# Kernel tuning notes

Measured on AMD Instinct MI355X. Metric: run time of the kernel, lower is better.

## Reference

```python
import jax, jax.numpy as jnp
import numpy as np

B, N, C, H = 4, 4096, 128, 4


def setup_inputs() -> dict:
    key = jax.random.key(0)
    ks = jax.random.split(key, 12)
    def rn(k, shape, s=0.02):
        return jax.random.normal(k, shape, jnp.float32) * s
    return dict(
        x=jax.random.normal(ks[0], (B, N, C), jnp.float32),
        p=jax.random.normal(ks[1], (B, N, 3), jnp.float32),
        fcl1_w=rn(ks[2], (C, C)), fcl1_b=jnp.zeros((C,), jnp.float32),
        # per-head (stacked over leading H axis) TransformerLayer params
        hq_w=rn(ks[3], (H, C, C)), hq_b=jnp.zeros((H, C), jnp.float32),
        hk_w=rn(ks[4], (H, C, C)), hk_b=jnp.zeros((H, C), jnp.float32),
        hv_w=rn(ks[5], (H, C, C)), hv_b=jnp.zeros((H, C), jnp.float32),
        pe1_w=rn(ks[6], (H, C, 3)), pe1_b=jnp.zeros((H, C), jnp.float32),  # Conv1d(3->C, k=1)
        pe2_w=rn(ks[7], (H, C, C)), pe2_b=jnp.zeros((H, C), jnp.float32),  # Conv1d(C->C, k=1)
        mh_w=rn(ks[8], (C, 4 * C)), mh_b=jnp.zeros((C,), jnp.float32),
        fcl2_w=rn(ks[9], (C, C)), fcl2_b=jnp.zeros((C,), jnp.float32),
    )


def reference(x, p, fcl1_w, fcl1_b, hq_w, hq_b, hk_w, hk_b, hv_w, hv_b,
              pe1_w, pe1_b, pe2_w, pe2_b, mh_w, mh_b, fcl2_w, fcl2_b):
    residual = x
    xf = x @ fcl1_w.T + fcl1_b  # fcl1
    scale = 1.0 / jnp.sqrt(jnp.asarray(C, jnp.float32))

    def head(qw, qb, kw, kb, vw, vb, p1w, p1b, p2w, p2b):
        # kernel-size-1 Conv1d == pointwise linear over coords
        pe = jax.nn.relu(jnp.einsum('bnd,cd->bnc', p, p1w) + p1b)
        pe = jnp.einsum('bnc,dc->bnd', pe, p2w) + p2b
        xh = xf + pe
        q = xh @ kw.T + kb  # note: original uses self.key for x_query
        k = xh @ qw.T + qb  # and self.query for x_key (name swap, kept faithful)
        v = xh @ vw.T + vb
        s = jax.nn.softmax(jnp.einsum('bnc,bmc->bnm', q, k) * scale, axis=-1)
        return jnp.einsum('bnm,bmc->bnc', s, v)

    outs = jax.vmap(head)(hq_w, hq_b, hk_w, hk_b, hv_w, hv_b,
                          pe1_w, pe1_b, pe2_w, pe2_b)  # [H,B,N,C]
    cat = jnp.moveaxis(outs, 0, 2).reshape(B, N, H * C)  # concat head1..head4 on last dim
    y = cat @ mh_w.T + mh_b
    y = y @ fcl2_w.T + fcl2_b
    mu = jnp.mean(y, axis=-1, keepdims=True)
    var = jnp.var(y, axis=-1, keepdims=True)
    y = (y - mu) / jnp.sqrt(var + 1e-5)  # torch.layer_norm, no affine
    return (y + residual, p)
```

## Files before the change

kernel.cpp:

```cpp
#include <hip/hip_runtime.h>
#include <hip/hip_bf16.h>

typedef __bf16 bf16;
typedef bf16 bf16x8 __attribute__((ext_vector_type(8)));
typedef float f32x4 __attribute__((ext_vector_type(4)));

static __device__ __forceinline__ f32x4 mfma16(bf16x8 a, bf16x8 b, f32x4 c) {
  return __builtin_amdgcn_mfma_f32_16x16x32_bf16(a, b, c, 0, 0, 0);
}

#define M_TOT 16384
#define CDIM 128
#define N_SEG 18
#define TOTAL_CONV 2511616

__global__ void probe_k(const unsigned short* __restrict__ xr, int* __restrict__ flag) {
  int wild = 0;
#pragma unroll
  for (int i = 0; i < 8; i++) {
    unsigned short w = xr[threadIdx.x * 8 + i];
    int e = (w >> 7) & 0xFF;
    if (e < 110 || e > 134) wild++;
  }
#pragma unroll
  for (int off = 1; off < 64; off <<= 1) wild += __shfl_xor(wild, off);
  if (threadIdx.x == 0) *flag = (wild > 64) ? 1 : 0;
}

struct ConvArgs { const void* src[N_SEG]; };

__global__ __launch_bounds__(256) void convall_k(ConvArgs a, bf16* __restrict__ dst,
                                                 void* __restrict__ outp,
                                                 const int* __restrict__ flag) {
  const int ends[N_SEG] = {2097152, 2146304, 2162688, 2162816, 2228352, 2228864,
                           2294400, 2294912, 2360448, 2360960, 2362496, 2363008,
                           2428544, 2429056, 2494592, 2495104, 2511488, 2511616};
  int i = blockIdx.x * 256 + threadIdx.x;
  if (i >= TOTAL_CONV) {
    int j = i - TOTAL_CONV;
    if (j < 49152) {
      if (*flag) ((float*)outp)[2097152 + j] = ((const float*)a.src[1])[j];
      else       ((bf16*)outp)[2097152 + j]  = ((const bf16*)a.src[1])[j];
    }
    return;
  }
  int s = 0;
  while (i >= ends[s]) s++;
  int j = i - (s ? ends[s - 1] : 0);
  if (*flag) dst[i] = (bf16)((const float*)a.src[s])[j];
  else       dst[i] = ((const bf16*)a.src[s])[j];
}

__global__ __launch_bounds__(256, 2) void pre_k(
    const bf16* __restrict__ x, const bf16* __restrict__ p,
    const bf16* __restrict__ f1w, const bf16* __restrict__ f1b,
    const bf16* __restrict__ pe1w, const bf16* __restrict__ pe1b,
    const bf16* __restrict__ pe2w, const bf16* __restrict__ pe2b,
    const bf16* __restrict__ Wq, const bf16* __restrict__ Bq,
    const bf16* __restrict__ Wk, const bf16* __restrict__ Bk,
    const bf16* __restrict__ Wv, const bf16* __restrict__ Bv,
    bf16* __restrict__ qo, bf16* __restrict__ ko, bf16* __restrict__ vo)
{
  const int lane = threadIdx.x & 63;
  const int wave = threadIdx.x >> 6;
  const int quad = lane >> 4;
  const int n15 = lane & 15;
  const int h = blockIdx.y;
  const int r0 = blockIdx.x * 128;
  const int wr = wave * 32;

  __shared__ bf16 xft[128][136];
  __shared__ bf16 pet[128][136];
  __shared__ bf16 pst[4][32][4];
  __shared__ bf16 wst[4][128][4];

  {
    f32x4 acc[2][8] = {};
#pragma unroll
    for (int kk = 0; kk < 4; kk++) {
      const int ka = kk * 32 + quad * 8;
      bf16x8 a0 = *(const bf16x8*)(x + (long)(r0 + wr + n15) * 128 + ka);
      bf16x8 a1 = *(const bf16x8*)(x + (long)(r0 + wr + 16 + n15) * 128 + ka);
#pragma unroll
      for (int ct = 0; ct < 8; ct++) {
        bf16x8 wf = *(const bf16x8*)(f1w + (long)(ct * 16 + n15) * 128 + ka);
        acc[0][ct] = mfma16(a0, wf, acc[0][ct]);
        acc[1][ct] = mfma16(a1, wf, acc[1][ct]);
      }
    }
#pragma unroll
    for (int g = 0; g < 2; g++)
#pragma unroll
      for (int ct = 0; ct < 8; ct++) {
        const int col = ct * 16 + n15;
        const float bv = (float)f1b[col];
#pragma unroll
        for (int r = 0; r < 4; r++)
          xft[wr + g * 16 + quad * 4 + r][col] = (bf16)(acc[g][ct][r] + bv);
      }
  }

  if (lane < 32) {
    const bf16* pr = p + (long)(r0 + wr + lane) * 3;
    pst[wave][lane][0] = pr[0]; pst[wave][lane][1] = pr[1]; pst[wave][lane][2] = pr[2];
  }
  for (int i = lane; i < 128; i += 64) {
    const bf16* wrp = pe1w + ((long)h * 128 + i) * 3;
    wst[wave][i][0] = wrp[0]; wst[wave][i][1] = wrp[1]; wst[wave][i][2] = wrp[2];
  }
#pragma unroll
  for (int cc = 0; cc < 2; cc++) {
    const int c = cc * 64 + lane;
    const float w0 = (float)wst[wave][c][0];
    const float w1 = (float)wst[wave][c][1];
    const float w2 = (float)wst[wave][c][2];
    const float bb = (float)pe1b[h * 128 + c];
    for (int rr = 0; rr < 32; rr++) {
      const float p0 = (float)pst[wave][rr][0];
      const float p1 = (float)pst[wave][rr][1];
      const float p2 = (float)pst[wave][rr][2];
      pet[wr + rr][c] = (bf16)fmaxf(p0 * w0 + p1 * w1 + p2 * w2 + bb, 0.f);
    }
  }

  {
    f32x4 acc[2][8] = {};
#pragma unroll
    for (int kk = 0; kk < 4; kk++) {
      const int ka = kk * 32 + quad * 8;
      bf16x8 a0 = *(const bf16x8*)&pet[wr + n15][ka];
      bf16x8 a1 = *(const bf16x8*)&pet[wr + 16 + n15][ka];
#pragma unroll
      for (int ct = 0; ct < 8; ct++) {
        bf16x8 wf = *(const bf16x8*)(pe2w + (long)h * 16384 + (long)(ct * 16 + n15) * 128 + ka);
        acc[0][ct] = mfma16(a0, wf, acc[0][ct]);
        acc[1][ct] = mfma16(a1, wf, acc[1][ct]);
      }
    }
#pragma unroll
    for (int g = 0; g < 2; g++)
#pragma unroll
      for (int ct = 0; ct < 8; ct++) {
        const int col = ct * 16 + n15;
        const float bv = (float)pe2b[h * 128 + col];
#pragma unroll
        for (int r = 0; r < 4; r++) {
          const int rl = wr + g * 16 + quad * 4 + r;
          xft[rl][col] = (bf16)(acc[g][ct][r] + bv + (float)xft[rl][col]);
        }
      }
  }

  bf16x8 af[2][4];
#pragma unroll
  for (int g = 0; g < 2; g++)
#pragma unroll
    for (int kk = 0; kk < 4; kk++)
      af[g][kk] = *(const bf16x8*)&xft[wr + g * 16 + n15][kk * 32 + quad * 8];

  const bf16* Ws[3] = {Wq, Wk, Wv};
  const bf16* Bs[3] = {Bq, Bk, Bv};
#pragma unroll
  for (int m = 0; m < 3; m++) {
    f32x4 acc[2][8] = {};
#pragma unroll
    for (int kk = 0; kk < 4; kk++) {
      const int ka = kk * 32 + quad * 8;
#pragma unroll
      for (int ct = 0; ct < 8; ct++) {
        bf16x8 wf = *(const bf16x8*)(Ws[m] + (long)h * 16384 + (long)(ct * 16 + n15) * 128 + ka);
        acc[0][ct] = mfma16(af[0][kk], wf, acc[0][ct]);
        acc[1][ct] = mfma16(af[1][kk], wf, acc[1][ct]);
      }
    }
    if (m < 2) {
      bf16* oz = (m == 0 ? qo : ko) + (long)h * 2097152;
#pragma unroll
      for (int g = 0; g < 2; g++)
#pragma unroll
        for (int ct = 0; ct < 8; ct++) {
          const int col = ct * 16 + n15;
          const float bv = (float)Bs[m][h * 128 + col];
#pragma unroll
          for (int r = 0; r < 4; r++)
            oz[(long)(r0 + wr + g * 16 + quad * 4 + r) * 128 + col] = (bf16)(acc[g][ct][r] + bv);
        }
    } else {
      bf16* vz = vo + (long)h * (128L * 16384);
#pragma unroll
      for (int g = 0; g < 2; g++)
#pragma unroll
        for (int ct = 0; ct < 8; ct++) {
          const int col = ct * 16 + n15;
          const float bv = (float)Bs[2][h * 128 + col];
#pragma unroll
          for (int r = 0; r < 4; r++)
            vz[(long)col * 16384 + (r0 + wr + g * 16 + quad * 4 + r)] = (bf16)(acc[g][ct][r] + bv);
        }
    }
  }
}

__global__ __launch_bounds__(256, 2) void attn_k(
    const bf16* __restrict__ Q, const bf16* __restrict__ Kg,
    const bf16* __restrict__ vT, bf16* __restrict__ cat)
{
  const int lane = threadIdx.x & 63;
  const int wave = threadIdx.x >> 6;
  const int quad = lane >> 4;
  const int n15 = lane & 15;
  const int b = blockIdx.y, h = blockIdx.z;
  const long qkBase = ((long)h * 4 + b) * 4096 * 128;
  const long vBase = (long)h * (128L * 16384) + (long)b * 4096;
  const int wrow = blockIdx.x * 128 + wave * 32;

  __shared__ bf16 Kt[128 * 128];
  __shared__ bf16 Vt[128 * 128];
  __shared__ bf16 Pt[4][16 * 128];

  const float scale = 0.08838834764831845f;
  bf16x8 qf[2][4];
#pragma unroll
  for (int g = 0; g < 2; g++)
#pragma unroll
    for (int kk = 0; kk < 4; kk++) {
      bf16x8 t = *(const bf16x8*)(Q + qkBase + (long)(wrow + g * 16 + n15) * 128 + kk * 32 + quad * 8);
#pragma unroll
      for (int j = 0; j < 8; j++) t[j] = (bf16)((float)t[j] * scale);
      qf[g][kk] = t;
    }

  f32x4 Om[2][8] = {};
  float l_part[2][4] = {};

  for (int kv0 = 0; kv0 < 4096; kv0 += 128) {
    __syncthreads();
    {
      const int rr = threadIdx.x >> 4;
      const int ch = threadIdx.x & 15;
#pragma unroll
      for (int i = 0; i < 8; i++) {
        const int row = rr + i * 16;
        *(bf16x8*)&Kt[row * 128 + ((ch ^ (row & 15)) * 8)] =
            *(const bf16x8*)(Kg + qkBase + (long)(kv0 + row) * 128 + ch * 8);
      }
#pragma unroll
      for (int i = 0; i < 8; i++) {
        const int c = rr + i * 16;
        *(bf16x8*)&Vt[c * 128 + ((ch ^ (c & 15)) * 8)] =
            *(const bf16x8*)(vT + vBase + (long)c * 16384 + kv0 + ch * 8);
      }
    }
    __syncthreads();

    f32x4 S[2][8] = {};
#pragma unroll
    for (int kk = 0; kk < 4; kk++) {
#pragma unroll
      for (int ct = 0; ct < 8; ct++) {
        const int row = ct * 16 + n15;
        bf16x8 kf = *(const bf16x8*)&Kt[row * 128 + (((kk * 4 + quad) ^ (row & 15)) * 8)];
        S[0][ct] = mfma16(qf[0][kk], kf, S[0][ct]);
        S[1][ct] = mfma16(qf[1][kk], kf, S[1][ct]);
      }
    }

    bf16x8 pf[2][4];
#pragma unroll
    for (int g = 0; g < 2; g++) {
#pragma unroll
      for (int ct = 0; ct < 8; ct++)
#pragma unroll
        for (int r = 0; r < 4; r++) {
          float e = __expf(S[g][ct][r]);
          l_part[g][r] += e;
          const int row = quad * 4 + r;
          const int kv = ct * 16 + n15;
          Pt[wave][row * 128 + (((kv >> 3) ^ row) * 8) + (kv & 7)] = (bf16)e;
        }
#pragma unroll
      for (int kk = 0; kk < 4; kk++)
        pf[g][kk] = *(const bf16x8*)&Pt[wave][n15 * 128 + (((kk * 4 + quad) ^ n15) * 8)];
    }

#pragma unroll
    for (int kk = 0; kk < 4; kk++) {
      bf16x8 vf[8];
#pragma unroll
      for (int ct = 0; ct < 8; ct++) {
        const int c = ct * 16 + n15;
        vf[ct] = *(const bf16x8*)&Vt[c * 128 + (((kk * 4 + quad) ^ (c & 15)) * 8)];
      }
#pragma unroll
      for (int g = 0; g < 2; g++)
#pragma unroll
        for (int ct = 0; ct < 8; ct++)
          Om[g][ct] = mfma16(pf[g][kk], vf[ct], Om[g][ct]);
    }
  }

#pragma unroll
  for (int g = 0; g < 2; g++) {
    float inv[4];
#pragma unroll
    for (int r = 0; r < 4; r++) {
      float s = l_part[g][r];
#pragma unroll
      for (int off = 1; off < 16; off <<= 1) s += __shfl_xor(s, off);
      inv[r] = 1.f / s;
    }
    const long ob = ((long)b * 4096 + wrow + g * 16 + quad * 4) * 512 + h * 128;
#pragma unroll
    for (int ct = 0; ct < 8; ct++)
#pragma unroll
      for (int r = 0; r < 4; r++)
        cat[ob + (long)r * 512 + ct * 16 + n15] = (bf16)(Om[g][ct][r] * inv[r]);
  }
}

__global__ __launch_bounds__(256) void tail_k(
    const bf16* __restrict__ cat,
    const bf16* __restrict__ mhw, const bf16* __restrict__ mhb,
    const bf16* __restrict__ f2w, const bf16* __restrict__ f2b,
    const void* __restrict__ xraw, void* __restrict__ outraw,
    const int* __restrict__ flag)
{
  const int lane = threadIdx.x & 63;
  const int wave = threadIdx.x >> 6;
  const int quad = lane >> 4;
  const int n15 = lane & 15;
  const int r0 = blockIdx.x * 64 + wave * 16;
  __shared__ bf16 y1t[64][136];

  f32x4 acc[8] = {};
  for (int k0 = 0; k0 < 512; k0 += 32) {
    const int ka = k0 + quad * 8;
    bf16x8 a0 = *(const bf16x8*)(cat + (long)(r0 + n15) * 512 + ka);
#pragma unroll
    for (int ct = 0; ct < 8; ct++) {
      bf16x8 wf = *(const bf16x8*)(mhw + (long)(ct * 16 + n15) * 512 + ka);
      acc[ct] = mfma16(a0, wf, acc[ct]);
    }
  }
#pragma unroll
  for (int ct = 0; ct < 8; ct++) {
    const float bv = (float)mhb[ct * 16 + n15];
#pragma unroll
    for (int r = 0; r < 4; r++)
      y1t[wave * 16 + quad * 4 + r][ct * 16 + n15] = (bf16)(acc[ct][r] + bv);
  }

  f32x4 acc2[8] = {};
  for (int k0 = 0; k0 < 128; k0 += 32) {
    const int ka = k0 + quad * 8;
    bf16x8 a0 = *(const bf16x8*)&y1t[wave * 16 + n15][ka];
#pragma unroll
    for (int ct = 0; ct < 8; ct++) {
      bf16x8 wf = *(const bf16x8*)(f2w + (long)(ct * 16 + n15) * 128 + ka);
      acc2[ct] = mfma16(a0, wf, acc2[ct]);
    }
  }

  float s1[4] = {}, s2[4] = {};
#pragma unroll
  for (int ct = 0; ct < 8; ct++) {
    const float bv = (float)f2b[ct * 16 + n15];
#pragma unroll
    for (int r = 0; r < 4; r++) {
      const float v = acc2[ct][r] + bv;
      acc2[ct][r] = v;
      s1[r] += v;
      s2[r] += v * v;
    }
  }
  float mu[4], inv[4];
#pragma unroll
  for (int r = 0; r < 4; r++) {
    float a = s1[r], b2 = s2[r];
#pragma unroll
    for (int off = 1; off < 16; off <<= 1) {
      a += __shfl_xor(a, off);
      b2 += __shfl_xor(b2, off);
    }
    mu[r] = a * (1.f / 128.f);
    const float var = fmaxf(b2 * (1.f / 128.f) - mu[r] * mu[r], 0.f);
    inv[r] = rsqrtf(var + 1e-5f);
  }

  const int isF32 = *flag;
#pragma unroll
  for (int ct = 0; ct < 8; ct++)
#pragma unroll
    for (int r = 0; r < 4; r++) {
      const long idx = (long)(r0 + quad * 4 + r) * 128 + ct * 16 + n15;
      const float resid = isF32 ? ((const float*)xraw)[idx]
                                : (float)((const bf16*)xraw)[idx];
      const float v = (acc2[ct][r] - mu[r]) * inv[r] + resid;
      if (isF32) ((float*)outraw)[idx] = v;
      else       ((bf16*)outraw)[idx] = (bf16)v;
    }
}

extern "C" void kernel_launch(void* const* d_in, const int* in_sizes, int n_in,
                              void* d_out, int out_size, void* d_ws, size_t ws_size,
                              hipStream_t stream)
{
  bf16* ws  = (bf16*)d_ws;
  bf16* q   = ws + 2097152;
  bf16* kb  = ws + 18874368;
  bf16* vt  = ws + 27262976;
  bf16* cat = ws + 35651584;
  const long AR = 44040192;
  int* flag = (int*)(ws + 46551808);

  static const int counts[N_SEG] = {2097152, 49152, 16384, 128, 65536, 512, 65536, 512,
                                    65536, 512, 1536, 512, 65536, 512, 65536, 512, 16384, 128};
  long offs[N_SEG]; long o = AR;
  for (int i = 0; i < N_SEG; i++) { offs[i] = o; o += counts[i]; }
  bf16* xc    = ws + offs[0];
  bf16* pc    = ws + offs[1];
  bf16* f1w   = ws + offs[2];
  bf16* f1b   = ws + offs[3];
  bf16* hqw   = ws + offs[4];
  bf16* hqb   = ws + offs[5];
  bf16* hkw   = ws + offs[6];
  bf16* hkb   = ws + offs[7];
  bf16* hvw   = ws + offs[8];
  bf16* hvb   = ws + offs[9];
  bf16* pe1w  = ws + offs[10];
  bf16* pe1b  = ws + offs[11];
  bf16* pe2w  = ws + offs[12];
  bf16* pe2b  = ws + offs[13];
  bf16* mhw   = ws + offs[14];
  bf16* mhb   = ws + offs[15];
  bf16* f2w   = ws + offs[16];
  bf16* f2b   = ws + offs[17];

  probe_k<<<dim3(1), dim3(64), 0, stream>>>((const unsigned short*)d_in[0], flag);
  ConvArgs ca;
  for (int i = 0; i < N_SEG; i++) ca.src[i] = d_in[i];
  convall_k<<<dim3((TOTAL_CONV + 49152 + 255) / 256), dim3(256), 0, stream>>>(ca, ws + AR, d_out, flag);

  dim3 blk(256);
  pre_k<<<dim3(128, 4), blk, 0, stream>>>(xc, pc, f1w, f1b, pe1w, pe1b, pe2w, pe2b,
                                          hkw, hkb, hqw, hqb, hvw, hvb, q, kb, vt);
  attn_k<<<dim3(32, 4, 4), blk, 0, stream>>>(q, kb, vt, cat);
  tail_k<<<dim3(256), blk, 0, stream>>>(cat, mhw, mhb, f2w, f2b, d_in[0], d_out, flag);
}
```

Baseline: 400.1 us.

## Split attention over two KV halves and merge partial sums in tail kernel

Attention now splits the KV range into two halves per query tile, doubling the grid and using smaller 64-wide KV tiles with less shared memory so more blocks fit per CU. Unnormalized partial outputs and row sums go to workspace, and the tail kernel adds the halves and normalizes while loading. The pre kernel is reworked to 64-row blocks, computes the pe1 conv with an MFMA, folds fcl1 into the pe2 accumulator, and writes transposed V through shared memory for coalesced stores. The cost is extra workspace traffic for the two partial outputs and the merge work in the tail kernel.

```diff
diff --git a/kernel.cpp b/kernel.cpp
--- a/kernel.cpp
+++ b/kernel.cpp
@@ -9,8 +9,6 @@
   return __builtin_amdgcn_mfma_f32_16x16x32_bf16(a, b, c, 0, 0, 0);
 }
 
-#define M_TOT 16384
-#define CDIM 128
 #define N_SEG 18
 #define TOTAL_CONV 2511616
 
@@ -51,7 +49,7 @@
   else       dst[i] = ((const bf16*)a.src[s])[j];
 }
 
-__global__ __launch_bounds__(256, 2) void pre_k(
+__global__ __launch_bounds__(256, 4) void pre_k(
     const bf16* __restrict__ x, const bf16* __restrict__ p,
     const bf16* __restrict__ f1w, const bf16* __restrict__ f1b,
     const bf16* __restrict__ pe1w, const bf16* __restrict__ pe1b,
@@ -66,157 +64,155 @@
   const int quad = lane >> 4;
   const int n15 = lane & 15;
   const int h = blockIdx.y;
-  const int r0 = blockIdx.x * 128;
-  const int wr = wave * 32;
-
-  __shared__ bf16 xft[128][136];
-  __shared__ bf16 pet[128][136];
-  __shared__ bf16 pst[4][32][4];
-  __shared__ bf16 wst[4][128][4];
+  const int r0 = blockIdx.x * 64;
+  const int wr = wave * 16;
+
+  __shared__ bf16 tile[9216];
+
+  f32x4 acc[8];
+  const f32x4 zz = {};
 
   {
-    f32x4 acc[2][8] = {};
+    bf16x8 ap = {};
+    if (quad == 0) {
+      const bf16* pr = p + (long)(r0 + wr + n15) * 3;
+      ap[0] = pr[0]; ap[1] = pr[1]; ap[2] = pr[2];
+    }
+#pragma unroll
+    for (int ct = 0; ct < 8; ct++) {
+      bf16x8 bw = {};
+      if (quad == 0) {
+        const bf16* wp = pe1w + ((long)h * 128 + ct * 16 + n15) * 3;
+        bw[0] = wp[0]; bw[1] = wp[1]; bw[2] = wp[2];
+      }
+      acc[ct] = mfma16(ap, bw, zz);
+    }
+#pragma unroll
+    for (int ct = 0; ct < 8; ct++) {
+      const int col = ct * 16 + n15;
+      const float bb = (float)pe1b[h * 128 + col];
+#pragma unroll
+      for (int r = 0; r < 4; r++)
+        tile[(wr + quad * 4 + r) * 136 + col] = (bf16)fmaxf(acc[ct][r] + bb, 0.f);
+    }
+  }
+
+#pragma unroll
+  for (int ct = 0; ct < 8; ct++) acc[ct] = zz;
+#pragma unroll
+  for (int kk = 0; kk < 4; kk++) {
+    const int ka = kk * 32 + quad * 8;
+    bf16x8 a0 = *(const bf16x8*)&tile[(wr + n15) * 136 + ka];
+#pragma unroll
+    for (int ct = 0; ct < 8; ct++) {
+      bf16x8 wf = *(const bf16x8*)(pe2w + (long)h * 16384 + (long)(ct * 16 + n15) * 128 + ka);
+      acc[ct] = mfma16(a0, wf, acc[ct]);
+    }
+  }
+#pragma unroll
+  for (int kk = 0; kk < 4; kk++) {
+    const int ka = kk * 32 + quad * 8;
+    bf16x8 a0 = *(const bf16x8*)(x + (long)(r0 + wr + n15) * 128 + ka);
+#pragma unroll
+    for (int ct = 0; ct < 8; ct++) {
+      bf16x8 wf = *(const bf16x8*)(f1w + (long)(ct * 16 + n15) * 128 + ka);
+      acc[ct] = mfma16(a0, wf, acc[ct]);
+    }
+  }
+#pragma unroll
+  for (int ct = 0; ct < 8; ct++) {
+    const int col = ct * 16 + n15;
+    const float bv = (float)pe2b[h * 128 + col] + (float)f1b[col];
+#pragma unroll
+    for (int r = 0; r < 4; r++)
+      tile[(wr + quad * 4 + r) * 136 + col] = (bf16)(acc[ct][r] + bv);
+  }
+
+  bf16x8 af[4];
+#pragma unroll
+  for (int kk = 0; kk < 4; kk++)
+    af[kk] = *(const bf16x8*)&tile[(wr + n15) * 136 + kk * 32 + quad * 8];
+
+#pragma unroll
+  for (int m = 0; m < 2; m++) {
+    f32x4 a2[8];
+#pragma unroll
+    for (int ct = 0; ct < 8; ct++) a2[ct] = zz;
+    const bf16* Wm = (m == 0) ? Wq : Wk;
 #pragma unroll
     for (int kk = 0; kk < 4; kk++) {
       const int ka = kk * 32 + quad * 8;
-      bf16x8 a0 = *(const bf16x8*)(x + (long)(r0 + wr + n15) * 128 + ka);
-      bf16x8 a1 = *(const bf16x8*)(x + (long)(r0 + wr + 16 + n15) * 128 + ka);
 #pragma unroll
       for (int ct = 0; ct < 8; ct++) {
-        bf16x8 wf = *(const bf16x8*)(f1w + (long)(ct * 16 + n15) * 128 + ka);
-        acc[0][ct] = mfma16(a0, wf, acc[0][ct]);
-        acc[1][ct] = mfma16(a1, wf, acc[1][ct]);
-      }
-    }
-#pragma unroll
-    for (int g = 0; g < 2; g++)
-#pragma unroll
-      for (int ct = 0; ct < 8; ct++) {
-        const int col = ct * 16 + n15;
-        const float bv = (float)f1b[col];
-#pragma unroll
-        for (int r = 0; r < 4; r++)
-          xft[wr + g * 16 + quad * 4 + r][col] = (bf16)(acc[g][ct][r] + bv);
-      }
-  }
-
-  if (lane < 32) {
-    const bf16* pr = p + (long)(r0 + wr + lane) * 3;
-    pst[wave][lane][0] = pr[0]; pst[wave][lane][1] = pr[1]; pst[wave][lane][2] = pr[2];
-  }
-  for (int i = lane; i < 128; i += 64) {
-    const bf16* wrp = pe1w + ((long)h * 128 + i) * 3;
-    wst[wave][i][0] = wrp[0]; wst[wave][i][1] = wrp[1]; wst[wave][i][2] = wrp[2];
-  }
-#pragma unroll
-  for (int cc = 0; cc < 2; cc++) {
-    const int c = cc * 64 + lane;
-    const float w0 = (float)wst[wave][c][0];
-    const float w1 = (float)wst[wave][c][1];
-    const float w2 = (float)wst[wave][c][2];
-    const float bb = (float)pe1b[h * 128 + c];
-    for (int rr = 0; rr < 32; rr++) {
-      const float p0 = (float)pst[wave][rr][0];
-      const float p1 = (float)pst[wave][rr][1];
-      const float p2 = (float)pst[wave][rr][2];
-      pet[wr + rr][c] = (bf16)fmaxf(p0 * w0 + p1 * w1 + p2 * w2 + bb, 0.f);
+        bf16x8 wf = *(const bf16x8*)(Wm + (long)h * 16384 + (long)(ct * 16 + n15) * 128 + ka);
+        a2[ct] = mfma16(af[kk], wf, a2[ct]);
+      }
+    }
+    bf16* oz = ((m == 0) ? qo : ko) + (long)h * 2097152;
+    const bf16* Bz = (m == 0) ? Bq : Bk;
+#pragma unroll
+    for (int ct = 0; ct < 8; ct++) {
+      const int col = ct * 16 + n15;
+      const float bv = (float)Bz[h * 128 + col];
+#pragma unroll
+      for (int r = 0; r < 4; r++)
+        oz[(long)(r0 + wr + quad * 4 + r) * 128 + col] = (bf16)(a2[ct][r] + bv);
     }
   }
 
   {
-    f32x4 acc[2][8] = {};
+    f32x4 a2[8];
+#pragma unroll
+    for (int ct = 0; ct < 8; ct++) a2[ct] = zz;
 #pragma unroll
     for (int kk = 0; kk < 4; kk++) {
       const int ka = kk * 32 + quad * 8;
-      bf16x8 a0 = *(const bf16x8*)&pet[wr + n15][ka];
-      bf16x8 a1 = *(const bf16x8*)&pet[wr + 16 + n15][ka];
 #pragma unroll
       for (int ct = 0; ct < 8; ct++) {
-        bf16x8 wf = *(const bf16x8*)(pe2w + (long)h * 16384 + (long)(ct * 16 + n15) * 128 + ka);
-        acc[0][ct] = mfma16(a0, wf, acc[0][ct]);
-        acc[1][ct] = mfma16(a1, wf, acc[1][ct]);
-      }
-    }
-#pragma unroll
-    for (int g = 0; g < 2; g++)
-#pragma unroll
-      for (int ct = 0; ct < 8; ct++) {
-        const int col = ct * 16 + n15;
-        const float bv = (float)pe2b[h * 128 + col];
-#pragma unroll
-        for (int r = 0; r < 4; r++) {
-          const int rl = wr + g * 16 + quad * 4 + r;
-          xft[rl][col] = (bf16)(acc[g][ct][r] + bv + (float)xft[rl][col]);
-        }
-      }
-  }
-
-  bf16x8 af[2][4];
-#pragma unroll
-  for (int g = 0; g < 2; g++)
-#pragma unroll
-    for (int kk = 0; kk < 4; kk++)
-      af[g][kk] = *(const bf16x8*)&xft[wr + g * 16 + n15][kk * 32 + quad * 8];
-
-  const bf16* Ws[3] = {Wq, Wk, Wv};
-  const bf16* Bs[3] = {Bq, Bk, Bv};
-#pragma unroll
-  for (int m = 0; m < 3; m++) {
-    f32x4 acc[2][8] = {};
-#pragma unroll
-    for (int kk = 0; kk < 4; kk++) {
-      const int ka = kk * 32 + quad * 8;
-#pragma unroll
-      for (int ct = 0; ct < 8; ct++) {
-        bf16x8 wf = *(const bf16x8*)(Ws[m] + (long)h * 16384 + (long)(ct * 16 + n15) * 128 + ka);
-        acc[0][ct] = mfma16(af[0][kk], wf, acc[0][ct]);
-        acc[1][ct] = mfma16(af[1][kk], wf, acc[1][ct]);
-      }
-    }
-    if (m < 2) {
-      bf16* oz = (m == 0 ? qo : ko) + (long)h * 2097152;
-#pragma unroll
-      for (int g = 0; g < 2; g++)
-#pragma unroll
-        for (int ct = 0; ct < 8; ct++) {
-          const int col = ct * 16 + n15;
-          const float bv = (float)Bs[m][h * 128 + col];
-#pragma unroll
-          for (int r = 0; r < 4; r++)
-            oz[(long)(r0 + wr + g * 16 + quad * 4 + r) * 128 + col] = (bf16)(acc[g][ct][r] + bv);
-        }
-    } else {
-      bf16* vz = vo + (long)h * (128L * 16384);
-#pragma unroll
-      for (int g = 0; g < 2; g++)
-#pragma unroll
-        for (int ct = 0; ct < 8; ct++) {
-          const int col = ct * 16 + n15;
-          const float bv = (float)Bs[2][h * 128 + col];
-#pragma unroll
-          for (int r = 0; r < 4; r++)
-            vz[(long)col * 16384 + (r0 + wr + g * 16 + quad * 4 + r)] = (bf16)(acc[g][ct][r] + bv);
-        }
-    }
-  }
-}
-
-__global__ __launch_bounds__(256, 2) void attn_k(
+        bf16x8 wf = *(const bf16x8*)(Wv + (long)h * 16384 + (long)(ct * 16 + n15) * 128 + ka);
+        a2[ct] = mfma16(af[kk], wf, a2[ct]);
+      }
+    }
+    __syncthreads();
+#pragma unroll
+    for (int ct = 0; ct < 8; ct++) {
+      const int col = ct * 16 + n15;
+      const float bv = (float)Bv[h * 128 + col];
+#pragma unroll
+      for (int r = 0; r < 4; r++)
+        tile[col * 72 + (wr + quad * 4 + r)] = (bf16)(a2[ct][r] + bv);
+    }
+    __syncthreads();
+    bf16* vz = vo + (long)h * 2097152;
+#pragma unroll
+    for (int i = 0; i < 16; i++) {
+      const int c = wave * 32 + i * 2 + (lane >> 5);
+      const int m2 = (lane & 31) * 2;
+      *(unsigned int*)&vz[(long)c * 16384 + r0 + m2] =
+          *(const unsigned int*)&tile[c * 72 + m2];
+    }
+  }
+}
+
+__global__ __launch_bounds__(256, 4) void attn_k(
     const bf16* __restrict__ Q, const bf16* __restrict__ Kg,
-    const bf16* __restrict__ vT, bf16* __restrict__ cat)
+    const bf16* __restrict__ vT, bf16* __restrict__ Op, float* __restrict__ ls)
 {
   const int lane = threadIdx.x & 63;
   const int wave = threadIdx.x >> 6;
   const int quad = lane >> 4;
   const int n15 = lane & 15;
+  const int qt = blockIdx.x >> 1;
+  const int half = blockIdx.x & 1;
   const int b = blockIdx.y, h = blockIdx.z;
   const long qkBase = ((long)h * 4 + b) * 4096 * 128;
   const long vBase = (long)h * (128L * 16384) + (long)b * 4096;
-  const int wrow = blockIdx.x * 128 + wave * 32;
-
-  __shared__ bf16 Kt[128 * 128];
-  __shared__ bf16 Vt[128 * 128];
-  __shared__ bf16 Pt[4][16 * 128];
+  const int wrow = qt * 128 + wave * 32;
+  const int kvStart = half * 2048;
+
+  __shared__ bf16 Kt[64 * 128];
+  __shared__ bf16 Vt[128 * 64];
+  __shared__ bf16 Pt[4][1024];
 
   const float scale = 0.08838834764831845f;
   bf16x8 qf[2][4];
@@ -233,63 +229,64 @@
   f32x4 Om[2][8] = {};
   float l_part[2][4] = {};
 
-  for (int kv0 = 0; kv0 < 4096; kv0 += 128) {
+  for (int kv0 = kvStart; kv0 < kvStart + 2048; kv0 += 64) {
     __syncthreads();
     {
       const int rr = threadIdx.x >> 4;
       const int ch = threadIdx.x & 15;
 #pragma unroll
-      for (int i = 0; i < 8; i++) {
+      for (int i = 0; i < 4; i++) {
         const int row = rr + i * 16;
-        *(bf16x8*)&Kt[row * 128 + ((ch ^ (row & 15)) * 8)] =
+        *(bf16x8*)&Kt[row * 128 + ((ch ^ rr) * 8)] =
             *(const bf16x8*)(Kg + qkBase + (long)(kv0 + row) * 128 + ch * 8);
       }
-#pragma unroll
-      for (int i = 0; i < 8; i++) {
-        const int c = rr + i * 16;
-        *(bf16x8*)&Vt[c * 128 + ((ch ^ (c & 15)) * 8)] =
-            *(const bf16x8*)(vT + vBase + (long)c * 16384 + kv0 + ch * 8);
+      const int vc = threadIdx.x >> 3;
+      const int vch = threadIdx.x & 7;
+#pragma unroll
+      for (int i = 0; i < 4; i++) {
+        const int c = vc + i * 32;
+        *(bf16x8*)&Vt[c * 64 + ((vch ^ (c & 7)) * 8)] =
+            *(const bf16x8*)(vT + vBase + (long)c * 16384 + kv0 + vch * 8);
       }
     }
     __syncthreads();
 
-    f32x4 S[2][8] = {};
+    f32x4 S[2][4] = {};
 #pragma unroll
     for (int kk = 0; kk < 4; kk++) {
 #pragma unroll
-      for (int ct = 0; ct < 8; ct++) {
-        const int row = ct * 16 + n15;
-        bf16x8 kf = *(const bf16x8*)&Kt[row * 128 + (((kk * 4 + quad) ^ (row & 15)) * 8)];
+      for (int ct = 0; ct < 4; ct++) {
+        bf16x8 kf = *(const bf16x8*)&Kt[(ct * 16 + n15) * 128 + (((kk * 4 + quad) ^ n15) * 8)];
         S[0][ct] = mfma16(qf[0][kk], kf, S[0][ct]);
         S[1][ct] = mfma16(qf[1][kk], kf, S[1][ct]);
       }
     }
 
-    bf16x8 pf[2][4];
+    bf16x8 pf[2][2];
 #pragma unroll
     for (int g = 0; g < 2; g++) {
 #pragma unroll
-      for (int ct = 0; ct < 8; ct++)
+      for (int ct = 0; ct < 4; ct++)
 #pragma unroll
         for (int r = 0; r < 4; r++) {
           float e = __expf(S[g][ct][r]);
           l_part[g][r] += e;
           const int row = quad * 4 + r;
           const int kv = ct * 16 + n15;
-          Pt[wave][row * 128 + (((kv >> 3) ^ row) * 8) + (kv & 7)] = (bf16)e;
+          Pt[wave][row * 64 + ((((kv >> 3) ^ (row & 7)) * 8)) + (kv & 7)] = (bf16)e;
         }
 #pragma unroll
-      for (int kk = 0; kk < 4; kk++)
-        pf[g][kk] = *(const bf16x8*)&Pt[wave][n15 * 128 + (((kk * 4 + quad) ^ n15) * 8)];
-    }
-
-#pragma unroll
-    for (int kk = 0; kk < 4; kk++) {
+      for (int kk = 0; kk < 2; kk++)
+        pf[g][kk] = *(const bf16x8*)&Pt[wave][n15 * 64 + (((kk * 4 + quad) ^ (n15 & 7)) * 8)];
+    }
+
+#pragma unroll
+    for (int kk = 0; kk < 2; kk++) {
       bf16x8 vf[8];
 #pragma unroll
       for (int ct = 0; ct < 8; ct++) {
         const int c = ct * 16 + n15;
-        vf[ct] = *(const bf16x8*)&Vt[c * 128 + (((kk * 4 + quad) ^ (c & 15)) * 8)];
+        vf[ct] = *(const bf16x8*)&Vt[c * 64 + (((kk * 4 + quad) ^ (c & 7)) * 8)];
       }
 #pragma unroll
       for (int g = 0; g < 2; g++)
@@ -301,25 +298,25 @@
 
 #pragma unroll
   for (int g = 0; g < 2; g++) {
-    float inv[4];
 #pragma unroll
     for (int r = 0; r < 4; r++) {
       float s = l_part[g][r];
 #pragma unroll
       for (int off = 1; off < 16; off <<= 1) s += __shfl_xor(s, off);
-      inv[r] = 1.f / s;
-    }
-    const long ob = ((long)b * 4096 + wrow + g * 16 + quad * 4) * 512 + h * 128;
+      if (n15 == 0)
+        ls[((long)half * 4 + h) * 16384 + b * 4096 + wrow + g * 16 + quad * 4 + r] = s;
+    }
+    const long ob = (long)half * 8388608 + (long)(b * 4096 + wrow + g * 16 + quad * 4) * 512 + h * 128;
 #pragma unroll
     for (int ct = 0; ct < 8; ct++)
 #pragma unroll
       for (int r = 0; r < 4; r++)
-        cat[ob + (long)r * 512 + ct * 16 + n15] = (bf16)(Om[g][ct][r] * inv[r]);
+        Op[ob + (long)r * 512 + ct * 16 + n15] = (bf16)Om[g][ct][r];
   }
 }
 
 __global__ __launch_bounds__(256) void tail_k(
-    const bf16* __restrict__ cat,
+    const bf16* __restrict__ Op, const float* __restrict__ ls,
     const bf16* __restrict__ mhw, const bf16* __restrict__ mhb,
     const bf16* __restrict__ f2w, const bf16* __restrict__ f2b,
     const void* __restrict__ xraw, void* __restrict__ outraw,
@@ -332,10 +329,24 @@
   const int r0 = blockIdx.x * 64 + wave * 16;
   __shared__ bf16 y1t[64][136];
 
+  float invA[4];
+#pragma unroll
+  for (int hh = 0; hh < 4; hh++) {
+    const float l0 = ls[(long)hh * 16384 + r0 + n15];
+    const float l1 = ls[(long)(4 + hh) * 16384 + r0 + n15];
+    invA[hh] = 1.f / (l0 + l1);
+  }
+
   f32x4 acc[8] = {};
   for (int k0 = 0; k0 < 512; k0 += 32) {
+    const int hh = k0 >> 7;
     const int ka = k0 + quad * 8;
-    bf16x8 a0 = *(const bf16x8*)(cat + (long)(r0 + n15) * 512 + ka);
+    bf16x8 v0 = *(const bf16x8*)(Op + (long)(r0 + n15) * 512 + ka);
+    bf16x8 v1 = *(const bf16x8*)(Op + 8388608L + (long)(r0 + n15) * 512 + ka);
+    bf16x8 a0;
+#pragma unroll
+    for (int j = 0; j < 8; j++)
+      a0[j] = (bf16)(((float)v0[j] + (float)v1[j]) * invA[hh]);
 #pragma unroll
     for (int ct = 0; ct < 8; ct++) {
       bf16x8 wf = *(const bf16x8*)(mhw + (long)(ct * 16 + n15) * 512 + ka);
@@ -406,12 +417,13 @@
                               hipStream_t stream)
 {
   bf16* ws  = (bf16*)d_ws;
-  bf16* q   = ws + 2097152;
-  bf16* kb  = ws + 18874368;
-  bf16* vt  = ws + 27262976;
-  bf16* cat = ws + 35651584;
-  const long AR = 44040192;
-  int* flag = (int*)(ws + 46551808);
+  bf16* q   = ws;
+  bf16* kb  = ws + 8388608;
+  bf16* vt  = ws + 16777216;
+  bf16* Op  = ws + 25165824;
+  float* lsb = (float*)(ws + 41943040);
+  const long AR = 42205184;
+  int* flag = (int*)(ws + 44720000);
 
   static const int counts[N_SEG] = {2097152, 49152, 16384, 128, 65536, 512, 65536, 512,
                                     65536, 512, 1536, 512, 65536, 512, 65536, 512, 16384, 128};
@@ -442,8 +454,8 @@
   convall_k<<<dim3((TOTAL_CONV + 49152 + 255) / 256), dim3(256), 0, stream>>>(ca, ws + AR, d_out, flag);
 
   dim3 blk(256);
-  pre_k<<<dim3(128, 4), blk, 0, stream>>>(xc, pc, f1w, f1b, pe1w, pe1b, pe2w, pe2b,
+  pre_k<<<dim3(256, 4), blk, 0, stream>>>(xc, pc, f1w, f1b, pe1w, pe1b, pe2w, pe2b,
                                           hkw, hkb, hqw, hqb, hvw, hvb, q, kb, vt);
-  attn_k<<<dim3(32, 4, 4), blk, 0, stream>>>(q, kb, vt, cat);
-  tail_k<<<dim3(256), blk, 0, stream>>>(cat, mhw, mhb, f2w, f2b, d_in[0], d_out, flag);
-}
+  attn_k<<<dim3(64, 4, 4), blk, 0, stream>>>(q, kb, vt, Op, lsb);
+  tail_k<<<dim3(256), blk, 0, stream>>>(Op, lsb, mhw, mhb, f2w, f2b, d_in[0], d_out, flag);
+}
```

Result: slower. 678.3 us (+69.5%).
